# Kernel optimization log

Measured on AMD Instinct MI355X. Metric: run time of the kernel, lower is better.

The kernel has to match this reference:

```python
import jax, jax.numpy as jnp
import numpy as np


def setup_inputs() -> dict:
    key = jax.random.key(0)
    ks = jax.random.split(key, 6)
    B, H, W, C = 4, 64, 64, 256
    D = 256 // 4  # inter_channel // 4
    return {
        "g": jax.random.normal(ks[0], (B, H, W, C), dtype=jnp.float32),
        "x": jax.random.normal(ks[1], (B, H, W, C), dtype=jnp.float32),
        "x_query": jax.random.normal(ks[2], (B, H, W, D), dtype=jnp.float32),
        "phi_g": jax.random.normal(ks[3], (B, H, W, D), dtype=jnp.float32),
        "x_value": jax.random.normal(ks[4], (B, H, W, C), dtype=jnp.float32),
        "k": jax.random.normal(ks[5], (1,), dtype=jnp.float32),
    }


def reference(g, x, x_query, phi_g, x_value, k):
    B, H, W, C = x.shape
    D = x_query.shape[-1]
    HW = H * W
    q = x_query.reshape(B, HW, D)
    pg = phi_g.reshape(B, HW, D)
    v = x_value.reshape(B, HW, C)
    # scale[b,i,j] = sum_d phi_g[b,i,d] * x_query[b,j,d]  -> (B, HW, HW)
    scale = jnp.einsum("bid,bjd->bij", pg, q)
    soft = jax.nn.softmax(scale, axis=-1)
    # scaled_value[b,i,c] = sum_j soft[b,i,j] * v[b,j,c]
    sv = jnp.einsum("bij,bjc->bic", soft, v).reshape(B, H, W, C)
    layero = k * sv + x
    return jnp.concatenate([layero, g], axis=3)
```

## Files before the change

### kernel.cpp

```cpp
#include <hip/hip_runtime.h>

#define N_  4096
#define D_  64
#define C_  256

typedef short bf16x8 __attribute__((ext_vector_type(8)));
typedef float f32x4  __attribute__((ext_vector_type(4)));

__device__ __forceinline__ unsigned short f2bf(float f) {
    union { float f; unsigned int i; } v; v.f = f;
    unsigned int r = v.i + 0x7fffu + ((v.i >> 16) & 1u);
    return (unsigned short)(r >> 16);
}

__global__ void prepass_kernel(const float* __restrict__ xq,
                               const float* __restrict__ pg,
                               const float* __restrict__ xv,
                               unsigned short* __restrict__ qbf,
                               unsigned short* __restrict__ pgbf,
                               unsigned short* __restrict__ vt2) {
    const int bid = blockIdx.x;
    const int t   = threadIdx.x;
    if (bid < 512) {
        const float* src = (bid < 256) ? xq : pg;
        unsigned short* dst = (bid < 256) ? qbf : pgbf;
        const int base = (bid & 255) * 1024 + t;
#pragma unroll
        for (int it = 0; it < 4; ++it) {
            const int i = base + it * 256;
            float4 v = ((const float4*)src)[i];
            ushort4 o;
            o.x = f2bf(v.x); o.y = f2bf(v.y); o.z = f2bf(v.z); o.w = f2bf(v.w);
            ((ushort4*)dst)[i] = o;
        }
        return;
    }
    const int lane = t & 63;
    const int w    = t >> 6;
    const int l15  = lane & 15;
    const int quad = lane >> 4;
    const int f    = (bid - 512) * 4 + w;
    const int b    = f >> 11;
    const int jt   = (f >> 6) & 31;
    const int cb   = (f >> 2) & 15;
    const int ks   = f & 3;
    const int c    = cb * 16 + l15;
    const int jb   = jt * 128 + ks * 32 + quad * 8;
    const float* src = xv + ((size_t)b * N_ + jb) * C_ + c;
    float v0 = src[0 * C_], v1 = src[1 * C_], v2 = src[2 * C_], v3 = src[3 * C_];
    float v4 = src[4 * C_], v5 = src[5 * C_], v6 = src[6 * C_], v7 = src[7 * C_];
    uint4 o;
    o.x = (unsigned)f2bf(v0) | ((unsigned)f2bf(v1) << 16);
    o.y = (unsigned)f2bf(v2) | ((unsigned)f2bf(v3) << 16);
    o.z = (unsigned)f2bf(v4) | ((unsigned)f2bf(v5) << 16);
    o.w = (unsigned)f2bf(v6) | ((unsigned)f2bf(v7) << 16);
    *(uint4*)(vt2 + (size_t)f * 512 + lane * 8) = o;
}

__global__ __launch_bounds__(512, 2) void attn_main(
    const float* __restrict__ g,  const float* __restrict__ x,
    const float* __restrict__ kk, float* __restrict__ out,
    const unsigned short* __restrict__ qbf,
    const unsigned short* __restrict__ pgbf,
    const unsigned short* __restrict__ vt2)
{
    __shared__ unsigned short p_lds[2][64][132];
    __shared__ float s_l[64];

    const int t    = threadIdx.x;
    const int lane = t & 63;
    const int w    = t >> 6;
    const int l15  = lane & 15;
    const int quad = lane >> 4;

    const int bid = blockIdx.x;
    const int b   = bid & 3;
    const int rg  = bid >> 2;
    const int i0  = rg * 64;
    const size_t rowbase = (size_t)b * N_ + i0;

    if (t < 64) s_l[t] = 0.f;

#pragma unroll
    for (int it = 0; it < 8; ++it) {
        const int row = it * 8 + w;
        const int c4  = lane * 4;
        const float4 gv = *(const float4*)(g + (rowbase + row) * C_ + c4);
        *(float4*)(out + (rowbase + row) * (2 * C_) + C_ + c4) = gv;
    }

    bf16x8 pgf[4][2];
#pragma unroll
    for (int mt = 0; mt < 4; ++mt)
#pragma unroll
        for (int ks = 0; ks < 2; ++ks)
            pgf[mt][ks] = *(const bf16x8*)(pgbf +
                (rowbase + mt * 16 + l15) * D_ + ks * 32 + quad * 8);

    f32x4 oacc[4][2];
#pragma unroll
    for (int mt = 0; mt < 4; ++mt) { oacc[mt][0] = (f32x4){0.f,0.f,0.f,0.f};
                                     oacc[mt][1] = (f32x4){0.f,0.f,0.f,0.f}; }
    float ls[4][4];
#pragma unroll
    for (int mt = 0; mt < 4; ++mt)
#pragma unroll
        for (int r = 0; r < 4; ++r) ls[mt][r] = 0.f;

    const unsigned short* qb  = qbf + (size_t)b * N_ * D_;
    const unsigned short* vtb = vt2 + (size_t)b * N_ * C_;

    bf16x8 qf[2];
#pragma unroll
    for (int ks = 0; ks < 2; ++ks)
        qf[ks] = *(const bf16x8*)(qb + (size_t)(w * 16 + l15) * D_ + ks * 32 + quad * 8);

    __syncthreads();

    for (int jt = 0; jt < 32; ++jt) {
        const int buf = jt & 1;
        const unsigned short* tbase = vtb + (size_t)jt * 32768;

        bf16x8 vf[4][2];
#pragma unroll
        for (int ks = 0; ks < 4; ++ks)
#pragma unroll
            for (int ctl = 0; ctl < 2; ++ctl)
                vf[ks][ctl] = *(const bf16x8*)(tbase +
                    (size_t)(((w * 2 + ctl) * 4) + ks) * 512 + lane * 8);

        f32x4 sacc[4];
#pragma unroll
        for (int mt = 0; mt < 4; ++mt) sacc[mt] = (f32x4){0.f,0.f,0.f,0.f};
#pragma unroll
        for (int ks = 0; ks < 2; ++ks)
#pragma unroll
            for (int mt = 0; mt < 4; ++mt)
                sacc[mt] = __builtin_amdgcn_mfma_f32_16x16x32_bf16(pgf[mt][ks], qf[ks], sacc[mt], 0, 0, 0);

#pragma unroll
        for (int mt = 0; mt < 4; ++mt)
#pragma unroll
            for (int r = 0; r < 4; ++r) {
                const float p = __expf(sacc[mt][r]);
                ls[mt][r] += p;
                p_lds[buf][mt * 16 + quad * 4 + r][w * 16 + l15] = f2bf(p);
            }
        __syncthreads();

        if (jt < 31) {
            const int jn = (jt + 1) * 128;
#pragma unroll
            for (int ks = 0; ks < 2; ++ks)
                qf[ks] = *(const bf16x8*)(qb +
                    (size_t)(jn + w * 16 + l15) * D_ + ks * 32 + quad * 8);
        }

#pragma unroll
        for (int ks = 0; ks < 4; ++ks) {
            union { bf16x8 f; uint2 u2[2]; } pa[4];
#pragma unroll
            for (int mt = 0; mt < 4; ++mt) {
                const unsigned short* prow = &p_lds[buf][mt * 16 + l15][ks * 32 + quad * 8];
                pa[mt].u2[0] = *(const uint2*)prow;
                pa[mt].u2[1] = *(const uint2*)(prow + 4);
            }
#pragma unroll
            for (int mt = 0; mt < 4; ++mt) {
                oacc[mt][0] = __builtin_amdgcn_mfma_f32_16x16x32_bf16(pa[mt].f, vf[ks][0], oacc[mt][0], 0, 0, 0);
                oacc[mt][1] = __builtin_amdgcn_mfma_f32_16x16x32_bf16(pa[mt].f, vf[ks][1], oacc[mt][1], 0, 0, 0);
            }
        }
    }

#pragma unroll
    for (int mt = 0; mt < 4; ++mt)
#pragma unroll
        for (int r = 0; r < 4; ++r) {
            float s = ls[mt][r];
            s += __shfl_xor(s, 1); s += __shfl_xor(s, 2);
            s += __shfl_xor(s, 4); s += __shfl_xor(s, 8);
            if (l15 == 0) atomicAdd(&s_l[mt * 16 + quad * 4 + r], s);
        }
    __syncthreads();

    const float kval = kk[0];
#pragma unroll
    for (int mt = 0; mt < 4; ++mt)
#pragma unroll
        for (int r = 0; r < 4; ++r) {
            const int m = mt * 16 + quad * 4 + r;
            const float linv = 1.f / s_l[m];
            const size_t row = rowbase + m;
#pragma unroll
            for (int ctl = 0; ctl < 2; ++ctl) {
                const int c = w * 32 + ctl * 16 + l15;
                out[row * (2 * C_) + c] = kval * (oacc[mt][ctl][r] * linv) + x[row * C_ + c];
            }
        }
}

#define ROWS 4
#define FNT  256
__global__ __launch_bounds__(FNT, 2) void attn_fallback(
    const float* __restrict__ g, const float* __restrict__ x,
    const float* __restrict__ xq, const float* __restrict__ pg,
    const float* __restrict__ xv, const float* __restrict__ kk,
    float* __restrict__ out)
{
    __shared__ __align__(16) float s_pg[ROWS][D_];
    __shared__ __align__(16) float s_sc[N_ * ROWS];
    __shared__ float s_rmax[4][ROWS];
    __shared__ float s_rsum[4][ROWS];

    const int t = threadIdx.x, lane = t & 63, w = t >> 6, blk = blockIdx.x;
    const int b = blk >> 10, i0 = (blk & 1023) * ROWS;
    const size_t rowbase = (size_t)b * N_ + i0;
    {
        const int r = t >> 6, cc = (t & 63) * 4;
        const float4 gv = *(const float4*)(g + (rowbase + r) * C_ + cc);
        *(float4*)(out + (rowbase + r) * (2 * C_) + C_ + cc) = gv;
    }
    { const int r = t >> 6, d = t & 63; s_pg[r][d] = pg[(rowbase + r) * D_ + d]; }
    __syncthreads();
    const float* qb = xq + (size_t)b * N_ * D_;
    float lmax[ROWS];
#pragma unroll
    for (int r = 0; r < ROWS; ++r) lmax[r] = -1e30f;
    for (int jj = 0; jj < N_ / FNT; ++jj) {
        const int j = t + jj * FNT;
        const float4* q4p = (const float4*)(qb + (size_t)j * D_);
        float s[ROWS] = {0.f, 0.f, 0.f, 0.f};
#pragma unroll
        for (int u = 0; u < D_ / 8; ++u) {
            const float4 qa = q4p[u * 2], qc = q4p[u * 2 + 1];
#pragma unroll
            for (int r = 0; r < ROWS; ++r) {
                const float4 pa = *(const float4*)&s_pg[r][u * 8];
                const float4 pb = *(const float4*)&s_pg[r][u * 8 + 4];
                s[r] += qa.x * pa.x + qa.y * pa.y + qa.z * pa.z + qa.w * pa.w
                      + qc.x * pb.x + qc.y * pb.y + qc.z * pb.z + qc.w * pb.w;
            }
        }
        *(float4*)&s_sc[j * ROWS] = make_float4(s[0], s[1], s[2], s[3]);
#pragma unroll
        for (int r = 0; r < ROWS; ++r) lmax[r] = fmaxf(lmax[r], s[r]);
    }
#pragma unroll
    for (int r = 0; r < ROWS; ++r) {
        float m = lmax[r];
        for (int o = 32; o > 0; o >>= 1) m = fmaxf(m, __shfl_down(m, o));
        if (lane == 0) s_rmax[w][r] = m;
    }
    __syncthreads();
    float bmax[ROWS];
#pragma unroll
    for (int r = 0; r < ROWS; ++r)
        bmax[r] = fmaxf(fmaxf(s_rmax[0][r], s_rmax[1][r]), fmaxf(s_rmax[2][r], s_rmax[3][r]));
    float lsum[ROWS] = {0.f, 0.f, 0.f, 0.f};
    for (int jj = 0; jj < N_ / FNT; ++jj) {
        const int j = t + jj * FNT;
        float4 s4 = *(const float4*)&s_sc[j * ROWS];
        s4.x = __expf(s4.x - bmax[0]); s4.y = __expf(s4.y - bmax[1]);
        s4.z = __expf(s4.z - bmax[2]); s4.w = __expf(s4.w - bmax[3]);
        *(float4*)&s_sc[j * ROWS] = s4;
        lsum[0] += s4.x; lsum[1] += s4.y; lsum[2] += s4.z; lsum[3] += s4.w;
    }
#pragma unroll
    for (int r = 0; r < ROWS; ++r) {
        float sm = lsum[r];
        for (int o = 32; o > 0; o >>= 1) sm += __shfl_down(sm, o);
        if (lane == 0) s_rsum[w][r] = sm;
    }
    __syncthreads();
    float rinv[ROWS];
#pragma unroll
    for (int r = 0; r < ROWS; ++r)
        rinv[r] = 1.f / (s_rsum[0][r] + s_rsum[1][r] + s_rsum[2][r] + s_rsum[3][r]);
    const int jg = lane >> 4;
    const int c0 = (w * 16 + (lane & 15)) * 4;
    const float* vb = xv + (size_t)b * N_ * C_;
    float acc[ROWS][4];
#pragma unroll
    for (int r = 0; r < ROWS; ++r)
#pragma unroll
        for (int q = 0; q < 4; ++q) acc[r][q] = 0.f;
#pragma unroll 4
    for (int jj = 0; jj < N_ / 4; ++jj) {
        const int j = jj * 4 + jg;
        const float4 p4 = *(const float4*)&s_sc[j * ROWS];
        const float4 v4 = *(const float4*)(vb + (size_t)j * C_ + c0);
        acc[0][0] += p4.x * v4.x; acc[0][1] += p4.x * v4.y; acc[0][2] += p4.x * v4.z; acc[0][3] += p4.x * v4.w;
        acc[1][0] += p4.y * v4.x; acc[1][1] += p4.y * v4.y; acc[1][2] += p4.y * v4.z; acc[1][3] += p4.y * v4.w;
        acc[2][0] += p4.z * v4.x; acc[2][1] += p4.z * v4.y; acc[2][2] += p4.z * v4.z; acc[2][3] += p4.z * v4.w;
        acc[3][0] += p4.w * v4.x; acc[3][1] += p4.w * v4.y; acc[3][2] += p4.w * v4.z; acc[3][3] += p4.w * v4.w;
    }
#pragma unroll
    for (int r = 0; r < ROWS; ++r)
#pragma unroll
        for (int q = 0; q < 4; ++q) {
            acc[r][q] += __shfl_xor(acc[r][q], 16);
            acc[r][q] += __shfl_xor(acc[r][q], 32);
        }
    const float kval = kk[0];
    if (lane < 16) {
        const int c = (w * 16 + lane) * 4;
#pragma unroll
        for (int r = 0; r < ROWS; ++r) {
            const float4 xv4 = *(const float4*)(x + (rowbase + r) * C_ + c);
            float4 ov;
            ov.x = kval * (acc[r][0] * rinv[r]) + xv4.x;
            ov.y = kval * (acc[r][1] * rinv[r]) + xv4.y;
            ov.z = kval * (acc[r][2] * rinv[r]) + xv4.z;
            ov.w = kval * (acc[r][3] * rinv[r]) + xv4.w;
            *(float4*)(out + (rowbase + r) * (2 * C_) + c) = ov;
        }
    }
}

extern "C" void kernel_launch(void* const* d_in, const int* in_sizes, int n_in,
                              void* d_out, int out_size, void* d_ws, size_t ws_size,
                              hipStream_t stream) {
    const float* g  = (const float*)d_in[0];
    const float* x  = (const float*)d_in[1];
    const float* xq = (const float*)d_in[2];
    const float* pg = (const float*)d_in[3];
    const float* xv = (const float*)d_in[4];
    const float* kk = (const float*)d_in[5];
    float* out = (float*)d_out;

    const int B = in_sizes[0] / (N_ * C_);
    const size_t qn = (size_t)B * N_ * D_;
    const size_t vn = (size_t)B * N_ * C_;
    const size_t need = (2 * qn + vn) * sizeof(unsigned short);

    if (B != 4 || ws_size < need) {
        attn_fallback<<<dim3(B * (N_ / ROWS)), FNT, 0, stream>>>(g, x, xq, pg, xv, kk, out);
        return;
    }

    unsigned short* qbf  = (unsigned short*)d_ws;
    unsigned short* pgbf = qbf + qn;
    unsigned short* vt2  = pgbf + qn;

    prepass_kernel<<<dim3(512 + B * 512), 256, 0, stream>>>(xq, pg, xv, qbf, pgbf, vt2);
    attn_main<<<dim3(B * (N_ / 64)), 512, 0, stream>>>(g, x, kk, out, qbf, pgbf, vt2);
}
```

Baseline: 157.1 us.

## Software-pipeline S and PV steps, transpose S MFMA, swizzle P in LDS

Restructures the main loop so the QK^T/exp step for tile j+1 overlaps the PV MFMA for tile j, with ping-pong register sets for Q and V fragments and one barrier per tile instead of serializing S then PV. The S MFMA operands are swapped, so each lane holds four consecutive key columns for one query row. P is then written as packed ushort4 into an XOR-swizzled unpadded LDS buffer and read back as full 128-bit loads, cutting bank conflicts and LDS instructions. Row-sum reduction is simplified accordingly. The double register sets raise VGPR pressure, which could spill or lower occupancy under the 512x2 launch bounds.

```diff
diff --git a/kernel.cpp b/kernel.cpp
--- a/kernel.cpp
+++ b/kernel.cpp
@@ -64,7 +64,7 @@
     const unsigned short* __restrict__ pgbf,
     const unsigned short* __restrict__ vt2)
 {
-    __shared__ unsigned short p_lds[2][64][132];
+    __shared__ unsigned short p_lds[2][64 * 128];
     __shared__ float s_l[64];
 
     const int t    = threadIdx.x;
@@ -72,6 +72,7 @@
     const int w    = t >> 6;
     const int l15  = lane & 15;
     const int quad = lane >> 4;
+    const int swz  = (l15 & 7) << 4;
 
     const int bid = blockIdx.x;
     const int b   = bid & 3;
@@ -91,97 +92,113 @@
 
     bf16x8 pgf[4][2];
 #pragma unroll
-    for (int mt = 0; mt < 4; ++mt)
+    for (int nt = 0; nt < 4; ++nt)
 #pragma unroll
         for (int ks = 0; ks < 2; ++ks)
-            pgf[mt][ks] = *(const bf16x8*)(pgbf +
-                (rowbase + mt * 16 + l15) * D_ + ks * 32 + quad * 8);
+            pgf[nt][ks] = *(const bf16x8*)(pgbf +
+                (rowbase + nt * 16 + l15) * D_ + ks * 32 + quad * 8);
 
     f32x4 oacc[4][2];
 #pragma unroll
     for (int mt = 0; mt < 4; ++mt) { oacc[mt][0] = (f32x4){0.f,0.f,0.f,0.f};
                                      oacc[mt][1] = (f32x4){0.f,0.f,0.f,0.f}; }
-    float ls[4][4];
-#pragma unroll
-    for (int mt = 0; mt < 4; ++mt)
-#pragma unroll
-        for (int r = 0; r < 4; ++r) ls[mt][r] = 0.f;
+    float ls[4] = {0.f, 0.f, 0.f, 0.f};
 
     const unsigned short* qb  = qbf + (size_t)b * N_ * D_;
     const unsigned short* vtb = vt2 + (size_t)b * N_ * C_;
-
-    bf16x8 qf[2];
-#pragma unroll
-    for (int ks = 0; ks < 2; ++ks)
-        qf[ks] = *(const bf16x8*)(qb + (size_t)(w * 16 + l15) * D_ + ks * 32 + quad * 8);
-
-    __syncthreads();
-
-    for (int jt = 0; jt < 32; ++jt) {
-        const int buf = jt & 1;
+    unsigned short* const pb0 = &p_lds[0][0];
+    unsigned short* const pb1 = &p_lds[1][0];
+
+    auto load_q = [&](bf16x8 (&qf)[2], int jt) {
+#pragma unroll
+        for (int ks = 0; ks < 2; ++ks)
+            qf[ks] = *(const bf16x8*)(qb +
+                (size_t)(jt * 128 + w * 16 + l15) * D_ + ks * 32 + quad * 8);
+    };
+    auto load_v = [&](bf16x8 (&vf)[4][2], int jt) {
         const unsigned short* tbase = vtb + (size_t)jt * 32768;
-
-        bf16x8 vf[4][2];
 #pragma unroll
         for (int ks = 0; ks < 4; ++ks)
 #pragma unroll
             for (int ctl = 0; ctl < 2; ++ctl)
                 vf[ks][ctl] = *(const bf16x8*)(tbase +
                     (size_t)(((w * 2 + ctl) * 4) + ks) * 512 + lane * 8);
-
+    };
+    auto s_step = [&](const bf16x8 (&qf)[2], unsigned short* pbuf) {
         f32x4 sacc[4];
 #pragma unroll
-        for (int mt = 0; mt < 4; ++mt) sacc[mt] = (f32x4){0.f,0.f,0.f,0.f};
+        for (int nt = 0; nt < 4; ++nt) sacc[nt] = (f32x4){0.f,0.f,0.f,0.f};
 #pragma unroll
         for (int ks = 0; ks < 2; ++ks)
 #pragma unroll
-            for (int mt = 0; mt < 4; ++mt)
-                sacc[mt] = __builtin_amdgcn_mfma_f32_16x16x32_bf16(pgf[mt][ks], qf[ks], sacc[mt], 0, 0, 0);
-
-#pragma unroll
-        for (int mt = 0; mt < 4; ++mt)
-#pragma unroll
-            for (int r = 0; r < 4; ++r) {
-                const float p = __expf(sacc[mt][r]);
-                ls[mt][r] += p;
-                p_lds[buf][mt * 16 + quad * 4 + r][w * 16 + l15] = f2bf(p);
+            for (int nt = 0; nt < 4; ++nt)
+                sacc[nt] = __builtin_amdgcn_mfma_f32_16x16x32_bf16(
+                    qf[ks], pgf[nt][ks], sacc[nt], 0, 0, 0);
+#pragma unroll
+        for (int nt = 0; nt < 4; ++nt) {
+            const float p0 = __expf(sacc[nt][0]);
+            const float p1 = __expf(sacc[nt][1]);
+            const float p2 = __expf(sacc[nt][2]);
+            const float p3 = __expf(sacc[nt][3]);
+            ls[nt] += (p0 + p1) + (p2 + p3);
+            ushort4 pk;
+            pk.x = f2bf(p0); pk.y = f2bf(p1); pk.z = f2bf(p2); pk.w = f2bf(p3);
+            const int wb = ((nt * 16 + l15) * 256 + (w * 16 + quad * 4) * 2) ^ swz;
+            *(ushort4*)((char*)pbuf + wb) = pk;
+        }
+    };
+    auto pv_step = [&](const bf16x8 (&vf)[4][2], const unsigned short* pbuf) {
+#pragma unroll
+        for (int ks = 0; ks < 4; ++ks) {
+            bf16x8 pa[4];
+#pragma unroll
+            for (int mt = 0; mt < 4; ++mt) {
+                const int rb = ((mt * 16 + l15) * 256 + (ks * 32 + quad * 8) * 2) ^ swz;
+                pa[mt] = *(const bf16x8*)((const char*)pbuf + rb);
             }
+#pragma unroll
+            for (int mt = 0; mt < 4; ++mt) {
+                oacc[mt][0] = __builtin_amdgcn_mfma_f32_16x16x32_bf16(pa[mt], vf[ks][0], oacc[mt][0], 0, 0, 0);
+                oacc[mt][1] = __builtin_amdgcn_mfma_f32_16x16x32_bf16(pa[mt], vf[ks][1], oacc[mt][1], 0, 0, 0);
+            }
+        }
+    };
+
+    bf16x8 qfA[2], qfB[2], vfA[4][2], vfB[4][2];
+
+    load_q(qfA, 0);
+    load_v(vfA, 0);
+    s_step(qfA, pb0);
+    load_q(qfB, 1);
+    __syncthreads();
+
+#pragma unroll 1
+    for (int jtp = 0; jtp < 15; ++jtp) {
+        const int jt0 = 2 * jtp;
+        load_v(vfB, jt0 + 1);
+        load_q(qfA, jt0 + 2);
+        s_step(qfB, pb1);
+        pv_step(vfA, pb0);
         __syncthreads();
-
-        if (jt < 31) {
-            const int jn = (jt + 1) * 128;
-#pragma unroll
-            for (int ks = 0; ks < 2; ++ks)
-                qf[ks] = *(const bf16x8*)(qb +
-                    (size_t)(jn + w * 16 + l15) * D_ + ks * 32 + quad * 8);
-        }
-
-#pragma unroll
-        for (int ks = 0; ks < 4; ++ks) {
-            union { bf16x8 f; uint2 u2[2]; } pa[4];
-#pragma unroll
-            for (int mt = 0; mt < 4; ++mt) {
-                const unsigned short* prow = &p_lds[buf][mt * 16 + l15][ks * 32 + quad * 8];
-                pa[mt].u2[0] = *(const uint2*)prow;
-                pa[mt].u2[1] = *(const uint2*)(prow + 4);
-            }
-#pragma unroll
-            for (int mt = 0; mt < 4; ++mt) {
-                oacc[mt][0] = __builtin_amdgcn_mfma_f32_16x16x32_bf16(pa[mt].f, vf[ks][0], oacc[mt][0], 0, 0, 0);
-                oacc[mt][1] = __builtin_amdgcn_mfma_f32_16x16x32_bf16(pa[mt].f, vf[ks][1], oacc[mt][1], 0, 0, 0);
-            }
-        }
-    }
-
-#pragma unroll
-    for (int mt = 0; mt < 4; ++mt)
-#pragma unroll
-        for (int r = 0; r < 4; ++r) {
-            float s = ls[mt][r];
-            s += __shfl_xor(s, 1); s += __shfl_xor(s, 2);
-            s += __shfl_xor(s, 4); s += __shfl_xor(s, 8);
-            if (l15 == 0) atomicAdd(&s_l[mt * 16 + quad * 4 + r], s);
-        }
+        load_v(vfA, jt0 + 2);
+        load_q(qfB, jt0 + 3);
+        s_step(qfA, pb0);
+        pv_step(vfB, pb1);
+        __syncthreads();
+    }
+    load_v(vfB, 31);
+    s_step(qfB, pb1);
+    pv_step(vfA, pb0);
+    __syncthreads();
+    pv_step(vfB, pb1);
+
+#pragma unroll
+    for (int nt = 0; nt < 4; ++nt) {
+        float s = ls[nt];
+        s += __shfl_xor(s, 16);
+        s += __shfl_xor(s, 32);
+        if (lane < 16) atomicAdd(&s_l[nt * 16 + lane], s);
+    }
     __syncthreads();
 
     const float kval = kk[0];
```

New measurement: 153.6 us. 1.02x faster.
